# Kernel tuning notes

Hardware: AMD Instinct MI355X
Metric: run time of the kernel (lower is better)

Reference implementation:

```python
import jax, jax.numpy as jnp
import numpy as np

B, L = 8, 16384
H = 64          # num_channel
N2 = 32         # s4_hidden_size // 2 complex conjugate-pair modes
DEPTH = 4       # model_depth
NLAYERS = 1 + DEPTH  # number of DSSM layers
EPS = 1e-5


def setup_inputs() -> dict:
    key = jax.random.key(0)
    ks = jax.random.split(key, 12)
    x = jax.random.normal(ks[0], (B, L), dtype=jnp.float32)
    # input linear 1 -> H
    w_in = jax.random.normal(ks[1], (H,), dtype=jnp.float32)
    b_in = jax.random.normal(ks[2], (H,), dtype=jnp.float32) * 0.1
    # hidden linears H -> H
    w_mid = jax.random.normal(ks[3], (DEPTH, H, H), dtype=jnp.float32) / np.sqrt(H)
    b_mid = jax.random.normal(ks[4], (DEPTH, H), dtype=jnp.float32) * 0.1
    # output linear H -> 1
    w_out = jax.random.normal(ks[5], (H,), dtype=jnp.float32) / np.sqrt(H)
    b_out = jax.random.normal(ks[6], (), dtype=jnp.float32) * 0.1
    # S4D / DSSM parameters (stacked over the 5 SSM layers)
    log_dt = (jax.random.uniform(ks[7], (NLAYERS, H), dtype=jnp.float32)
              * (np.log(0.1) - np.log(0.001)) + np.log(0.001))
    log_A_real = jnp.log(0.5 * jnp.ones((NLAYERS, H, N2), dtype=jnp.float32))
    A_imag = jnp.pi * jnp.broadcast_to(jnp.arange(N2, dtype=jnp.float32), (NLAYERS, H, N2))
    C_re = jax.random.normal(ks[8], (NLAYERS, H, N2), dtype=jnp.float32)
    C_im = jax.random.normal(ks[9], (NLAYERS, H, N2), dtype=jnp.float32)
    D = jax.random.normal(ks[10], (NLAYERS, H), dtype=jnp.float32)
    return {"x": x, "w_in": w_in, "b_in": b_in, "w_mid": w_mid, "b_mid": b_mid,
            "w_out": w_out, "b_out": b_out, "log_dt": log_dt,
            "log_A_real": log_A_real, "A_imag": A_imag,
            "C_re": C_re, "C_im": C_im, "D": D}


def _dssm(u, log_dt, log_A_real, A_imag, C_re, C_im, D):
    # u: [B, H, L]; diagonal SSM applied as FFT convolution (S4D ZOH kernel)
    Lq = u.shape[-1]
    dt = jnp.exp(log_dt)                      # [H]
    A = -jnp.exp(log_A_real) + 1j * A_imag    # [H, N2]
    dtA = A * dt[:, None]                     # [H, N2]
    C_eff = (C_re + 1j * C_im) * (jnp.exp(dtA) - 1.0) / A
    # Vandermonde: exp(dtA * l) for l in [0, L)
    V = jnp.exp(dtA[:, :, None] * jnp.arange(Lq, dtype=jnp.float32))  # [H, N2, L]
    k = 2.0 * jnp.einsum('hn,hnl->hl', C_eff, V).real                # [H, L]
    uf = jnp.fft.rfft(u, n=2 * Lq)
    kf = jnp.fft.rfft(k, n=2 * Lq)
    y = jnp.fft.irfft(uf * kf, n=2 * Lq)[..., :Lq]
    return y + u * D[:, None]


def reference(x, w_in, b_in, w_mid, b_mid, w_out, b_out,
              log_dt, log_A_real, A_imag, C_re, C_im, D):
    # side chain: Abs -> Decibel -> Linear(1,H) -> tanh -> [DSSM -> tanh] ...
    s = 20.0 * jnp.log10(jnp.abs(x) + EPS)            # [B, L]
    h = jnp.tanh(s[..., None] * w_in + b_in)          # [B, L, H]
    h = jnp.tanh(_dssm(h.transpose(0, 2, 1), log_dt[0], log_A_real[0],
                       A_imag[0], C_re[0], C_im[0], D[0]).transpose(0, 2, 1))
    for i in range(DEPTH):
        h = jnp.tanh(jnp.einsum('blh,oh->blo', h, w_mid[i]) + b_mid[i])
        j = i + 1
        h = jnp.tanh(_dssm(h.transpose(0, 2, 1), log_dt[j], log_A_real[j],
                           A_imag[j], C_re[j], C_im[j], D[j]).transpose(0, 2, 1))
    g = jnp.einsum('blh,h->bl', h, w_out) + b_out      # [B, L]
    g = jnp.power(10.0, g / 20.0)                      # Amplitude (dB -> linear)
    return x * g
```

## Files before the change

kernel.cpp:

```cpp
#include <hip/hip_runtime.h>
#include <math.h>

#define Bq 8
#define Lq 16384
#define Hq 64
#define N2q 32
#define NLAYERSq 5

typedef _Float16 f16x8 __attribute__((ext_vector_type(8)));
typedef _Float16 f16x4 __attribute__((ext_vector_type(4)));
typedef float    f32x4 __attribute__((ext_vector_type(4)));

#define MFMA16F(a, b, c) __builtin_amdgcn_mfma_f32_16x16x32_f16(a, b, c, 0, 0, 0)

#define UT_OFF    0
#define SF_OFF    49152
#define SMEM_SZ   81920
#define YST_OFF   0
#define SF(row, c) ((row) * 128 + ((c) ^ ((row) & 31)))

#define WT_OFF_B   0
#define WP_OFF_B   163840
#define A2_OFF_B   (163840 + 5242880)
#define W16_OFF_B  (163840 + 5242880 + 15728640)
#define U_OFF_B    (163840 + 5242880 + 15728640 + 32768)

__device__ __forceinline__ float fast_tanh(float y) {
    float e = __expf(2.0f * y);
    return 1.0f - 2.0f * __builtin_amdgcn_rcpf(e + 1.0f);
}

__global__ __launch_bounds__(256)
void k_prep(const float* __restrict__ log_dt, const float* __restrict__ log_A_real,
            const float* __restrict__ A_imag, const float* __restrict__ C_re,
            const float* __restrict__ C_im, const float* __restrict__ Dvec,
            const float* __restrict__ w_mid,
            float* __restrict__ wT_tab, _Float16* __restrict__ Wp,
            _Float16* __restrict__ A2, _Float16* __restrict__ W16) {
    __shared__ float Pr[129][33], Pi[129][33];
    __shared__ float cre[32], cim[32], Kv[128];
    __shared__ double sdAr[32], sdAi[32];
    const int ph = blockIdx.x;
    const int tid = threadIdx.x;

    if (ph < 256 && tid < 64) {
        int e = ph * 64 + tid;
        W16[e] = (_Float16)w_mid[e];
    }

    if (tid < 32) {
        int n = tid;
        int pidx = ph * N2q + n;
        double dt  = exp((double)log_dt[ph]);
        double aRe = -exp((double)log_A_real[pidx]);
        double aIm = (double)A_imag[pidx];
        double dAr = aRe * dt, dAi = aIm * dt;
        sdAr[n] = dAr; sdAi[n] = dAi;
        double er  = exp(dAr);
        double wre = er * cos(dAi), wim = er * sin(dAi);
        double Er = wre - 1.0, Ei = wim;
        double inv = 1.0 / (aRe * aRe + aIm * aIm);
        double Fr = (Er * aRe + Ei * aIm) * inv;
        double Fi = (Ei * aRe - Er * aIm) * inv;
        double Cr = (double)C_re[pidx], Ci = (double)C_im[pidx];
        cre[n] = (float)(2.0 * (Cr * Fr - Ci * Fi));
        cim[n] = (float)(2.0 * (Cr * Fi + Ci * Fr));
        double qr = wre, qi = wim;
        #pragma unroll
        for (int s = 0; s < 7; s++) {
            double nr = qr * qr - qi * qi;
            qi = 2.0 * qr * qi; qr = nr;
        }
        float wTr = (float)qr, wTi = (float)qi;
        #pragma unroll
        for (int s = 0; s < 3; s++) {
            double nr = qr * qr - qi * qi;
            qi = 2.0 * qr * qi; qr = nr;
        }
        float* wt = wT_tab + ph * 128 + n * 4;
        wt[0] = wTr; wt[1] = wTi; wt[2] = (float)qr; wt[3] = (float)qi;
    }
    __syncthreads();

    const double TWO_PI  = 6.2831853071795864769;
    const double INV_2PI = 0.15915494309189533577;
    for (int e = tid; e < 129 * 32; e += 256) {
        int j = e >> 5, n = e & 31;
        double phd = (double)j * sdAi[n];
        double r   = fma(-TWO_PI, nearbyint(phd * INV_2PI), phd);
        float  mag = __expf((float)((double)j * sdAr[n]));
        float  rf  = (float)r;
        Pr[j][n] = mag * cosf(rf);
        Pi[j][n] = mag * sinf(rf);
    }
    __syncthreads();

    if (tid < 128) {
        int d = tid;
        float s = 0.f;
        #pragma unroll 8
        for (int n = 0; n < 32; n++)
            s += cre[n] * Pr[d][n] - cim[n] * Pi[d][n];
        if (d == 0) s += Dvec[ph];
        Kv[d] = s;
    }
    __syncthreads();

    _Float16* wpb = Wp + (size_t)ph * 8192;
    for (int e = tid; e < 8192; e += 256) {
        int kk = e >> 7, l = e & 127;
        float v = (kk < 32) ? Pr[127 - l][kk] : Pi[127 - l][kk - 32];
        wpb[e] = (_Float16)v;
    }
    _Float16* a2b = A2 + (size_t)ph * 24576;
    for (int e = tid; e < 24576; e += 256) {
        int m = e / 192, k = e - m * 192;
        float v;
        if (k < 128) {
            v = (k <= m) ? Kv[m - k] : 0.f;
        } else {
            int kk = k - 128, n2 = kk & 31;
            float pr = Pr[m + 1][n2], pi2 = Pi[m + 1][n2];
            v = (kk < 32) ? (cre[n2] * pr - cim[n2] * pi2)
                          : -(cre[n2] * pi2 + cim[n2] * pr);
        }
        a2b[e] = (_Float16)v;
    }
}

__global__ __launch_bounds__(512, 4)
void k_scan(const float* __restrict__ x, _Float16* __restrict__ u16,
            const _Float16* __restrict__ Wp_all, const _Float16* __restrict__ A2_all,
            const float* __restrict__ wT_all, int layer,
            const float* __restrict__ w_in, const float* __restrict__ b_in) {
    extern __shared__ char smem[];
    _Float16* UT = (_Float16*)(smem + UT_OFF);
    float*    Sf = (float*)(smem + SF_OFF);
    float*   yst = (float*)(smem + YST_OFF);

    const int bh = blockIdx.x;
    const int h  = bh & 63;
    const int tid = threadIdx.x;
    const int lane = tid & 63;
    const int wave = tid >> 6;
    const int ph = layer * 64 + h;
    const _Float16* Wp = Wp_all + (size_t)ph * 8192;
    const _Float16* A2 = A2_all + (size_t)ph * 24576;
    const float* wT4 = wT_all + ph * 128;
    _Float16* uu = u16 + ((size_t)bh << 14);

    const int rA = lane & 15;
    const int qA = lane >> 4;

    if (layer == 0) {
        const float* xb = x + ((size_t)(bh >> 6) << 14);
        const float wi = w_in[h], bi = b_in[h];
        for (int it = 0; it < 4; ++it) {
            int flat8 = (it * 512 + tid) * 8;
            int n = flat8 >> 7, k = flat8 & 127;
            float4 a = *(const float4*)(xb + flat8);
            float4 b = *(const float4*)(xb + flat8 + 4);
            float f[8] = {a.x, a.y, a.z, a.w, b.x, b.y, b.z, b.w};
            f16x8 hv;
            #pragma unroll
            for (int j = 0; j < 8; j++) {
                float s = 6.0205999132796239f * __log2f(fabsf(f[j]) + 1e-5f);
                hv[j] = (_Float16)fast_tanh(fmaf(s, wi, bi));
            }
            int kb = (k * 2) ^ ((n & 7) << 4);
            *(f16x8*)((char*)UT + n * 384 + kb) = hv;
        }
    } else {
        for (int it = 0; it < 4; ++it) {
            int flat8 = (it * 512 + tid) * 8;
            int n = flat8 >> 7, k = flat8 & 127;
            f16x8 hv = *(const f16x8*)(uu + flat8);
            int kb = (k * 2) ^ ((n & 7) << 4);
            *(f16x8*)((char*)UT + n * 384 + kb) = hv;
        }
    }
    __syncthreads();

    {
        f32x4 acc1[4];
        #pragma unroll
        for (int nt = 0; nt < 4; nt++) acc1[nt] = (f32x4){0.f, 0.f, 0.f, 0.f};
        const int mt1 = wave & 3;
        const int nh  = (wave >> 2) * 4;
        for (int ks = 0; ks < 4; ks++) {
            f16x8 af = *(const f16x8*)(Wp + (mt1 * 16 + rA) * 128 + ks * 32 + qA * 8);
            #pragma unroll
            for (int nt = 0; nt < 4; nt++) {
                int n = (nh + nt) * 16 + rA;
                int kb = (ks * 64 + qA * 16) ^ ((n & 7) << 4);
                f16x8 bv = *(const f16x8*)((char*)UT + n * 384 + kb);
                acc1[nt] = MFMA16F(af, bv, acc1[nt]);
            }
        }
        #pragma unroll
        for (int nt = 0; nt < 4; nt++) {
            int c = (nh + nt) * 16 + rA;
            #pragma unroll
            for (int r = 0; r < 4; r++)
                Sf[SF(mt1 * 16 + qA * 4 + r, c)] = acc1[nt][r];
        }
    }
    __syncthreads();

    {
        const int sn = tid >> 4;
        const int ss = tid & 15;
        const float wTr = wT4[sn * 4 + 0], wTi = wT4[sn * 4 + 1];
        float fr[8], fi[8];
        #pragma unroll
        for (int i = 0; i < 8; i++) {
            fr[i] = Sf[SF(sn,      ss * 8 + i)];
            fi[i] = Sf[SF(sn + 32, ss * 8 + i)];
        }
        float Tr = 0.f, Ti = 0.f;
        #pragma unroll
        for (int i = 0; i < 8; i++) {
            float nTr = fmaf(wTr, Tr, fmaf(-wTi, Ti, fr[i]));
            Ti = fmaf(wTr, Ti, fmaf(wTi, Tr, fi[i]));
            Tr = nTr;
        }
        float gr = wT4[sn * 4 + 2], gi = wT4[sn * 4 + 3];
        #pragma unroll
        for (int s = 0; s < 4; s++) {
            float pr = __shfl_up(Tr, 1 << s, 16);
            float pi = __shfl_up(Ti, 1 << s, 16);
            if (ss >= (1 << s)) {
                Tr = fmaf(gr, pr, fmaf(-gi, pi, Tr));
                Ti = fmaf(gr, pi, fmaf(gi, pr, Ti));
            }
            float ngr = fmaf(gr, gr, -gi * gi);
            gi = 2.f * gr * gi; gr = ngr;
        }
        float Er_ = __shfl_up(Tr, 1, 16);
        float Ei_ = __shfl_up(Ti, 1, 16);
        if (ss == 0) { Er_ = 0.f; Ei_ = 0.f; }
        float Gr = Er_, Gi = Ei_;
        #pragma unroll
        for (int i = 0; i < 8; i++) {
            Sf[SF(sn,      ss * 8 + i)] = Gr;
            Sf[SF(sn + 32, ss * 8 + i)] = Gi;
            float nGr = fmaf(wTr, Gr, fmaf(-wTi, Gi, fr[i]));
            Gi = fmaf(wTr, Gi, fmaf(wTi, Gr, fi[i]));
            Gr = nGr;
        }
    }
    __syncthreads();

    for (int e = tid; e < 8192; e += 512) {
        int kk = e >> 7, c = e & 127;
        float v = Sf[SF(kk, c)];
        int kb = (256 + kk * 2) ^ ((c & 7) << 4);
        *(_Float16*)((char*)UT + c * 384 + kb) = (_Float16)v;
    }
    __syncthreads();

    f32x4 acc[8];
    #pragma unroll
    for (int nt = 0; nt < 8; nt++) acc[nt] = (f32x4){0.f, 0.f, 0.f, 0.f};
    for (int ks = 0; ks < 6; ks++) {
        f16x8 a0 = *(const f16x8*)(A2 + (wave * 16 + rA) * 192 + ks * 32 + qA * 8);
        #pragma unroll
        for (int nt = 0; nt < 8; nt++) {
            int n = nt * 16 + rA;
            int kb = (ks * 64 + qA * 16) ^ ((n & 7) << 4);
            f16x8 bv = *(const f16x8*)((char*)UT + n * 384 + kb);
            acc[nt] = MFMA16F(a0, bv, acc[nt]);
        }
    }
    __syncthreads();

    {
        int m_base = wave * 16 + qA * 4;
        #pragma unroll
        for (int nt = 0; nt < 8; nt++) {
            int c = nt * 16 + rA;
            float4 o;
            o.x = fast_tanh(acc[nt][0]);
            o.y = fast_tanh(acc[nt][1]);
            o.z = fast_tanh(acc[nt][2]);
            o.w = fast_tanh(acc[nt][3]);
            *(float4*)(yst + c * 132 + m_base) = o;
        }
    }
    __syncthreads();
    for (int e = tid; e < 2048; e += 512) {
        int c = e >> 4, l8 = e & 15;
        float4 v0 = *(const float4*)(yst + c * 132 + l8 * 8);
        float4 v1 = *(const float4*)(yst + c * 132 + l8 * 8 + 4);
        f16x8 hv;
        hv[0] = (_Float16)v0.x; hv[1] = (_Float16)v0.y;
        hv[2] = (_Float16)v0.z; hv[3] = (_Float16)v0.w;
        hv[4] = (_Float16)v1.x; hv[5] = (_Float16)v1.y;
        hv[6] = (_Float16)v1.z; hv[7] = (_Float16)v1.w;
        *(f16x8*)(uu + c * 128 + l8 * 8) = hv;
    }
}

__global__ __launch_bounds__(256, 4)
void k_linear(_Float16* __restrict__ uio, const _Float16* __restrict__ W16,
              const float* __restrict__ bias) {
    __shared__ __align__(16) char lmem[33792];
    _Float16* Ul  = (_Float16*)lmem;
    _Float16* yst = (_Float16*)lmem;

    const int b   = blockIdx.y;
    const int l0  = blockIdx.x * 256;
    const int tid = threadIdx.x;
    const int lane = tid & 63;
    const int wave = tid >> 6;
    const int rA = lane & 15;
    const int qA = lane >> 4;

    _Float16* ub = uio + ((size_t)b << 20) + l0;

    for (int it = 0; it < 4; ++it) {
        int g  = it * 256 + tid;
        int hp = g >> 5;
        int l8 = g & 31;
        f16x8 v0 = *(const f16x8*)(ub + (size_t)(hp * 2)     * Lq + l8 * 8);
        f16x8 v1 = *(const f16x8*)(ub + (size_t)(hp * 2 + 1) * Lq + l8 * 8);
        const unsigned short* p0 = (const unsigned short*)&v0;
        const unsigned short* p1 = (const unsigned short*)&v1;
        int sw = (l8 & 7) << 4;
        #pragma unroll
        for (int j = 0; j < 8; j++) {
            unsigned int pk = (unsigned int)p0[j] | ((unsigned int)p1[j] << 16);
            *(unsigned int*)((char*)Ul + (l8 * 8 + j) * 128 + ((hp * 4) ^ sw)) = pk;
        }
    }
    __syncthreads();

    f32x4 acc[16];
    #pragma unroll
    for (int nt = 0; nt < 16; nt++) acc[nt] = (f32x4){0.f, 0.f, 0.f, 0.f};
    const _Float16* Wrow = W16 + (wave * 16 + rA) * 64;
    #pragma unroll
    for (int kf = 0; kf < 2; kf++) {
        f16x8 af = *(const f16x8*)(Wrow + kf * 32 + qA * 8);
        #pragma unroll
        for (int nt = 0; nt < 16; nt++) {
            int n = nt * 16 + rA;
            int sw = ((n >> 3) & 7) << 4;
            f16x8 bv = *(const f16x8*)((char*)Ul + n * 128 + ((kf * 64 + qA * 16) ^ sw));
            acc[nt] = MFMA16F(af, bv, acc[nt]);
        }
    }
    __syncthreads();

    {
        int ob = wave * 16 + qA * 4;
        float bo0 = bias[ob], bo1 = bias[ob + 1], bo2 = bias[ob + 2], bo3 = bias[ob + 3];
        #pragma unroll
        for (int nt = 0; nt < 16; nt++) {
            int l = nt * 16 + rA;
            yst[(ob + 0) * 264 + l] = (_Float16)fast_tanh(acc[nt][0] + bo0);
            yst[(ob + 1) * 264 + l] = (_Float16)fast_tanh(acc[nt][1] + bo1);
            yst[(ob + 2) * 264 + l] = (_Float16)fast_tanh(acc[nt][2] + bo2);
            yst[(ob + 3) * 264 + l] = (_Float16)fast_tanh(acc[nt][3] + bo3);
        }
    }
    __syncthreads();
    for (int it = 0; it < 8; ++it) {
        int e = it * 256 + tid;
        int o = e >> 5, l8 = e & 31;
        f16x8 hv = *(const f16x8*)(yst + o * 264 + l8 * 8);
        *(f16x8*)(ub + (size_t)o * Lq + l8 * 8) = hv;
    }
}

__global__ __launch_bounds__(256)
void k_out(const _Float16* __restrict__ u16, const float* __restrict__ x,
           const float* __restrict__ w_out, const float* __restrict__ b_out,
           float* __restrict__ out) {
    int idx = blockIdx.x * 256 + threadIdx.x;
    int b = idx >> 14;
    int l = idx & (Lq - 1);
    const _Float16* up = u16 + ((size_t)b << 20) + l;
    float acc = 0.f;
    #pragma unroll 8
    for (int hh = 0; hh < 64; ++hh)
        acc = fmaf(w_out[hh], (float)up[(size_t)hh << 14], acc);
    float g = acc + b_out[0];
    out[idx] = x[idx] * exp2f(g * 0.16609640474436812f);
}

extern "C" void kernel_launch(void* const* d_in, const int* in_sizes, int n_in,
                              void* d_out, int out_size, void* d_ws, size_t ws_size,
                              hipStream_t stream) {
    const float* x          = (const float*)d_in[0];
    const float* w_in       = (const float*)d_in[1];
    const float* b_in       = (const float*)d_in[2];
    const float* w_mid      = (const float*)d_in[3];
    const float* b_mid      = (const float*)d_in[4];
    const float* w_out      = (const float*)d_in[5];
    const float* b_out      = (const float*)d_in[6];
    const float* log_dt     = (const float*)d_in[7];
    const float* log_A_real = (const float*)d_in[8];
    const float* A_imag     = (const float*)d_in[9];
    const float* C_re       = (const float*)d_in[10];
    const float* C_im       = (const float*)d_in[11];
    const float* Dv         = (const float*)d_in[12];

    char* ws = (char*)d_ws;
    float*     wT_tab = (float*)(ws + WT_OFF_B);
    _Float16*  Wp     = (_Float16*)(ws + WP_OFF_B);
    _Float16*  A2     = (_Float16*)(ws + A2_OFF_B);
    _Float16*  W16    = (_Float16*)(ws + W16_OFF_B);
    _Float16*  u16    = (_Float16*)(ws + U_OFF_B);
    float* out = (float*)d_out;

    hipFuncSetAttribute((const void*)k_scan,
                        hipFuncAttributeMaxDynamicSharedMemorySize, SMEM_SZ);

    k_prep<<<NLAYERSq * Hq, 256, 0, stream>>>(log_dt, log_A_real, A_imag,
                                              C_re, C_im, Dv, w_mid,
                                              wT_tab, Wp, A2, W16);
    for (int layer = 0; layer < NLAYERSq; layer++) {
        if (layer > 0)
            k_linear<<<dim3(Lq / 256, Bq), 256, 0, stream>>>(
                u16, W16 + (size_t)(layer - 1) * Hq * Hq, b_mid + (size_t)(layer - 1) * Hq);
        k_scan<<<Bq * Hq, 512, SMEM_SZ, stream>>>(x, u16, Wp, A2, wT_tab, layer,
                                                  w_in, b_in);
    }
    k_out<<<(Bq * Lq) / 256, 256, 0, stream>>>(u16, x, w_out, b_out, out);
}
```

Measured before the change: 184.3 us.

## Halve scan block size, store scan state in fp16 transposed LDS layout

```diff
diff --git a/kernel.cpp b/kernel.cpp
--- a/kernel.cpp
+++ b/kernel.cpp
@@ -14,10 +14,9 @@
 #define MFMA16F(a, b, c) __builtin_amdgcn_mfma_f32_16x16x32_f16(a, b, c, 0, 0, 0)
 
 #define UT_OFF    0
-#define SF_OFF    49152
-#define SMEM_SZ   81920
+#define SS_OFF    32768
+#define SMEM_SZ   50176
 #define YST_OFF   0
-#define SF(row, c) ((row) * 128 + ((c) ^ ((row) & 31)))
 
 #define WT_OFF_B   0
 #define WP_OFF_B   163840
@@ -73,7 +72,7 @@
         }
         float wTr = (float)qr, wTi = (float)qi;
         #pragma unroll
-        for (int s = 0; s < 3; s++) {
+        for (int s = 0; s < 4; s++) {
             double nr = qr * qr - qi * qi;
             qi = 2.0 * qr * qi; qr = nr;
         }
@@ -128,15 +127,16 @@
     }
 }
 
-__global__ __launch_bounds__(512, 4)
+__global__ __launch_bounds__(256, 3)
 void k_scan(const float* __restrict__ x, _Float16* __restrict__ u16,
             const _Float16* __restrict__ Wp_all, const _Float16* __restrict__ A2_all,
             const float* __restrict__ wT_all, int layer,
             const float* __restrict__ w_in, const float* __restrict__ b_in) {
     extern __shared__ char smem[];
-    _Float16* UT = (_Float16*)(smem + UT_OFF);
-    float*    Sf = (float*)(smem + SF_OFF);
-    float*   yst = (float*)(smem + YST_OFF);
+    char* UT = smem + UT_OFF;
+    char* Sf = smem + SS_OFF;
+    char* St = smem + SS_OFF;
+    char* yst = smem + YST_OFF;
 
     const int bh = blockIdx.x;
     const int h  = bh & 63;
@@ -155,8 +155,8 @@
     if (layer == 0) {
         const float* xb = x + ((size_t)(bh >> 6) << 14);
         const float wi = w_in[h], bi = b_in[h];
-        for (int it = 0; it < 4; ++it) {
-            int flat8 = (it * 512 + tid) * 8;
+        for (int it = 0; it < 8; ++it) {
+            int flat8 = (it * 256 + tid) * 8;
             int n = flat8 >> 7, k = flat8 & 127;
             float4 a = *(const float4*)(xb + flat8);
             float4 b = *(const float4*)(xb + flat8 + 4);
@@ -167,68 +167,69 @@
                 float s = 6.0205999132796239f * __log2f(fabsf(f[j]) + 1e-5f);
                 hv[j] = (_Float16)fast_tanh(fmaf(s, wi, bi));
             }
-            int kb = (k * 2) ^ ((n & 7) << 4);
-            *(f16x8*)((char*)UT + n * 384 + kb) = hv;
+            *(f16x8*)(UT + n * 256 + ((k * 2) ^ ((n & 7) << 4))) = hv;
         }
     } else {
-        for (int it = 0; it < 4; ++it) {
-            int flat8 = (it * 512 + tid) * 8;
+        for (int it = 0; it < 8; ++it) {
+            int flat8 = (it * 256 + tid) * 8;
             int n = flat8 >> 7, k = flat8 & 127;
             f16x8 hv = *(const f16x8*)(uu + flat8);
-            int kb = (k * 2) ^ ((n & 7) << 4);
-            *(f16x8*)((char*)UT + n * 384 + kb) = hv;
+            *(f16x8*)(UT + n * 256 + ((k * 2) ^ ((n & 7) << 4))) = hv;
         }
     }
     __syncthreads();
 
     {
-        f32x4 acc1[4];
-        #pragma unroll
-        for (int nt = 0; nt < 4; nt++) acc1[nt] = (f32x4){0.f, 0.f, 0.f, 0.f};
-        const int mt1 = wave & 3;
-        const int nh  = (wave >> 2) * 4;
+        f32x4 acc1[8];
+        #pragma unroll
+        for (int nt = 0; nt < 8; nt++) acc1[nt] = (f32x4){0.f, 0.f, 0.f, 0.f};
         for (int ks = 0; ks < 4; ks++) {
-            f16x8 af = *(const f16x8*)(Wp + (mt1 * 16 + rA) * 128 + ks * 32 + qA * 8);
-            #pragma unroll
-            for (int nt = 0; nt < 4; nt++) {
-                int n = (nh + nt) * 16 + rA;
-                int kb = (ks * 64 + qA * 16) ^ ((n & 7) << 4);
-                f16x8 bv = *(const f16x8*)((char*)UT + n * 384 + kb);
+            f16x8 af = *(const f16x8*)(Wp + (wave * 16 + rA) * 128 + ks * 32 + qA * 8);
+            #pragma unroll
+            for (int nt = 0; nt < 8; nt++) {
+                int n = nt * 16 + rA;
+                f16x8 bv = *(const f16x8*)(UT + n * 256 + ((ks * 64 + qA * 16) ^ ((n & 7) << 4)));
                 acc1[nt] = MFMA16F(af, bv, acc1[nt]);
             }
         }
         #pragma unroll
-        for (int nt = 0; nt < 4; nt++) {
-            int c = (nh + nt) * 16 + rA;
+        for (int nt = 0; nt < 8; nt++) {
+            int c = nt * 16 + rA;
             #pragma unroll
             for (int r = 0; r < 4; r++)
-                Sf[SF(mt1 * 16 + qA * 4 + r, c)] = acc1[nt][r];
+                *(_Float16*)(Sf + (wave * 16 + qA * 4 + r) * 272 + c * 2) = (_Float16)acc1[nt][r];
         }
     }
     __syncthreads();
 
     {
-        const int sn = tid >> 4;
-        const int ss = tid & 15;
+        const int sn = tid >> 3;
+        const int ss = tid & 7;
         const float wTr = wT4[sn * 4 + 0], wTi = wT4[sn * 4 + 1];
-        float fr[8], fi[8];
-        #pragma unroll
-        for (int i = 0; i < 8; i++) {
-            fr[i] = Sf[SF(sn,      ss * 8 + i)];
-            fi[i] = Sf[SF(sn + 32, ss * 8 + i)];
+        float fr[16], fi[16];
+        {
+            f16x8 a0 = *(const f16x8*)(Sf + sn * 272 + ss * 32);
+            f16x8 a1 = *(const f16x8*)(Sf + sn * 272 + ss * 32 + 16);
+            f16x8 b0 = *(const f16x8*)(Sf + (sn + 32) * 272 + ss * 32);
+            f16x8 b1 = *(const f16x8*)(Sf + (sn + 32) * 272 + ss * 32 + 16);
+            #pragma unroll
+            for (int j = 0; j < 8; j++) {
+                fr[j] = (float)a0[j]; fr[j + 8] = (float)a1[j];
+                fi[j] = (float)b0[j]; fi[j + 8] = (float)b1[j];
+            }
         }
         float Tr = 0.f, Ti = 0.f;
         #pragma unroll
-        for (int i = 0; i < 8; i++) {
+        for (int i = 0; i < 16; i++) {
             float nTr = fmaf(wTr, Tr, fmaf(-wTi, Ti, fr[i]));
             Ti = fmaf(wTr, Ti, fmaf(wTi, Tr, fi[i]));
             Tr = nTr;
         }
         float gr = wT4[sn * 4 + 2], gi = wT4[sn * 4 + 3];
         #pragma unroll
-        for (int s = 0; s < 4; s++) {
-            float pr = __shfl_up(Tr, 1 << s, 16);
-            float pi = __shfl_up(Ti, 1 << s, 16);
+        for (int s = 0; s < 3; s++) {
+            float pr = __shfl_up(Tr, 1 << s, 8);
+            float pi = __shfl_up(Ti, 1 << s, 8);
             if (ss >= (1 << s)) {
                 Tr = fmaf(gr, pr, fmaf(-gi, pi, Tr));
                 Ti = fmaf(gr, pi, fmaf(gi, pr, Ti));
@@ -236,14 +237,17 @@
             float ngr = fmaf(gr, gr, -gi * gi);
             gi = 2.f * gr * gi; gr = ngr;
         }
-        float Er_ = __shfl_up(Tr, 1, 16);
-        float Ei_ = __shfl_up(Ti, 1, 16);
+        float Er_ = __shfl_up(Tr, 1, 8);
+        float Ei_ = __shfl_up(Ti, 1, 8);
         if (ss == 0) { Er_ = 0.f; Ei_ = 0.f; }
+        __syncthreads();
         float Gr = Er_, Gi = Ei_;
         #pragma unroll
-        for (int i = 0; i < 8; i++) {
-            Sf[SF(sn,      ss * 8 + i)] = Gr;
-            Sf[SF(sn + 32, ss * 8 + i)] = Gi;
+        for (int i = 0; i < 16; i++) {
+            int c = ss * 16 + i;
+            int sw = (c & 7) << 4;
+            *(_Float16*)(St + c * 128 + ((sn * 2) ^ sw))        = (_Float16)Gr;
+            *(_Float16*)(St + c * 128 + (((sn + 32) * 2) ^ sw)) = (_Float16)Gi;
             float nGr = fmaf(wTr, Gr, fmaf(-wTi, Gi, fr[i]));
             Gi = fmaf(wTr, Gi, fmaf(wTi, Gr, fi[i]));
             Gr = nGr;
@@ -251,52 +255,55 @@
     }
     __syncthreads();
 
-    for (int e = tid; e < 8192; e += 512) {
-        int kk = e >> 7, c = e & 127;
-        float v = Sf[SF(kk, c)];
-        int kb = (256 + kk * 2) ^ ((c & 7) << 4);
-        *(_Float16*)((char*)UT + c * 384 + kb) = (_Float16)v;
-    }
-    __syncthreads();
-
-    f32x4 acc[8];
+    f32x4 acc[2][8];
     #pragma unroll
-    for (int nt = 0; nt < 8; nt++) acc[nt] = (f32x4){0.f, 0.f, 0.f, 0.f};
-    for (int ks = 0; ks < 6; ks++) {
-        f16x8 a0 = *(const f16x8*)(A2 + (wave * 16 + rA) * 192 + ks * 32 + qA * 8);
-        #pragma unroll
-        for (int nt = 0; nt < 8; nt++) {
-            int n = nt * 16 + rA;
-            int kb = (ks * 64 + qA * 16) ^ ((n & 7) << 4);
-            f16x8 bv = *(const f16x8*)((char*)UT + n * 384 + kb);
-            acc[nt] = MFMA16F(a0, bv, acc[nt]);
-        }
-    }
-    __syncthreads();
-
-    {
-        int m_base = wave * 16 + qA * 4;
+    for (int mi = 0; mi < 2; mi++)
+        #pragma unroll
+        for (int nt = 0; nt < 8; nt++) acc[mi][nt] = (f32x4){0.f, 0.f, 0.f, 0.f};
+    #pragma unroll
+    for (int mi = 0; mi < 2; mi++) {
+        const _Float16* Arow = A2 + ((wave * 2 + mi) * 16 + rA) * 192;
+        for (int ks = 0; ks < 4; ks++) {
+            f16x8 af = *(const f16x8*)(Arow + ks * 32 + qA * 8);
+            #pragma unroll
+            for (int nt = 0; nt < 8; nt++) {
+                int n = nt * 16 + rA;
+                f16x8 bv = *(const f16x8*)(UT + n * 256 + ((ks * 64 + qA * 16) ^ ((n & 7) << 4)));
+                acc[mi][nt] = MFMA16F(af, bv, acc[mi][nt]);
+            }
+        }
+        #pragma unroll
+        for (int ks2 = 0; ks2 < 2; ks2++) {
+            f16x8 af = *(const f16x8*)(Arow + 128 + ks2 * 32 + qA * 8);
+            #pragma unroll
+            for (int nt = 0; nt < 8; nt++) {
+                int c = nt * 16 + rA;
+                f16x8 bv = *(const f16x8*)(St + c * 128 + ((ks2 * 64 + qA * 16) ^ ((c & 7) << 4)));
+                acc[mi][nt] = MFMA16F(af, bv, acc[mi][nt]);
+            }
+        }
+    }
+    __syncthreads();
+
+    #pragma unroll
+    for (int mi = 0; mi < 2; mi++) {
+        int m0 = (wave * 2 + mi) * 16 + qA * 4;
         #pragma unroll
         for (int nt = 0; nt < 8; nt++) {
             int c = nt * 16 + rA;
-            float4 o;
-            o.x = fast_tanh(acc[nt][0]);
-            o.y = fast_tanh(acc[nt][1]);
-            o.z = fast_tanh(acc[nt][2]);
-            o.w = fast_tanh(acc[nt][3]);
-            *(float4*)(yst + c * 132 + m_base) = o;
-        }
-    }
-    __syncthreads();
-    for (int e = tid; e < 2048; e += 512) {
+            f16x4 o;
+            o[0] = (_Float16)fast_tanh(acc[mi][nt][0]);
+            o[1] = (_Float16)fast_tanh(acc[mi][nt][1]);
+            o[2] = (_Float16)fast_tanh(acc[mi][nt][2]);
+            o[3] = (_Float16)fast_tanh(acc[mi][nt][3]);
+            *(f16x4*)(yst + c * 272 + m0 * 2) = o;
+        }
+    }
+    __syncthreads();
+    for (int it = 0; it < 8; ++it) {
+        int e = it * 256 + tid;
         int c = e >> 4, l8 = e & 15;
-        float4 v0 = *(const float4*)(yst + c * 132 + l8 * 8);
-        float4 v1 = *(const float4*)(yst + c * 132 + l8 * 8 + 4);
-        f16x8 hv;
-        hv[0] = (_Float16)v0.x; hv[1] = (_Float16)v0.y;
-        hv[2] = (_Float16)v0.z; hv[3] = (_Float16)v0.w;
-        hv[4] = (_Float16)v1.x; hv[5] = (_Float16)v1.y;
-        hv[6] = (_Float16)v1.z; hv[7] = (_Float16)v1.w;
+        f16x8 hv = *(const f16x8*)(yst + c * 272 + l8 * 16);
         *(f16x8*)(uu + c * 128 + l8 * 8) = hv;
     }
 }
@@ -424,7 +431,7 @@
         if (layer > 0)
             k_linear<<<dim3(Lq / 256, Bq), 256, 0, stream>>>(
                 u16, W16 + (size_t)(layer - 1) * Hq * Hq, b_mid + (size_t)(layer - 1) * Hq);
-        k_scan<<<Bq * Hq, 512, SMEM_SZ, stream>>>(x, u16, Wp, A2, wT_tab, layer,
+        k_scan<<<Bq * Hq, 256, SMEM_SZ, stream>>>(x, u16, Wp, A2, wT_tab, layer,
                                                   w_in, b_in);
     }
     k_out<<<(Bq * Lq) / 256, 256, 0, stream>>>(u16, x, w_out, b_out, out);
```

Measured after the change: 176.7 us. 1.04x faster.
